# Performance work log

Hardware: AMD Instinct MI355X
Metric: run time of the kernel (lower is better)

## Reference

```python
import jax, jax.numpy as jnp
import numpy as np

LOG2PI = float(np.log(2.0 * np.pi))
BN_EPS = 1e-5


def _spn_layer(x, scopes, mean, std, sum_w, bn_w, bn_b):
    """Vectorized SPNLayer of SPNNeurons.
    x:      [B, F]
    scopes: [O, F] int, per-neuron permutation of feature indices
    mean/std: [O, F//2, n_mv, 2] gaussian leaf params (pairs of features)
    sum_w:  [O, F//2, n_mv] sum-node mixture weights (softmax-normalized)
    bn_w, bn_b: [O] batchnorm affine params (training-mode batch stats)
    returns [B, O]
    """
    B = x.shape[0]
    O, P, M, _ = mean.shape
    # gather permuted features and group into pairs: [B, O, P, 2]
    xp = x[:, scopes].reshape(B, O, P, 2)
    # gaussian leaf log-likelihoods: [B, O, P, M, 2]
    z = (xp[:, :, :, None, :] - mean) / std
    ll = -0.5 * (z * z) - jnp.log(std) - 0.5 * LOG2PI
    # product node over each pair: [B, O, P, M]
    prod = ll.sum(axis=-1)
    # sum node: weighted mixture in log domain: [B, O, P]
    logw = jax.nn.log_softmax(sum_w, axis=-1)
    s = jax.nn.logsumexp(prod + logw, axis=-1)
    # root product node over all pairs: [B, O]
    out = s.sum(axis=-1)
    # BatchNorm1d (training mode, biased variance)
    mu = out.mean(axis=0)
    var = ((out - mu) ** 2).mean(axis=0)
    return (out - mu) / jnp.sqrt(var + BN_EPS) * bn_w + bn_b


def setup_inputs() -> dict:
    key = jax.random.key(0)
    ks = jax.random.split(key, 12)
    B, F_IN = 32768, 784
    H1, O1, O2, OUT = 32, 16, 10, 10
    n_mv = 2

    rng = np.random.RandomState(0)
    scopes1 = jnp.asarray(np.stack([rng.permutation(H1) for _ in range(O1)]), dtype=jnp.int32)
    scopes2 = jnp.asarray(np.stack([rng.permutation(O1) for _ in range(O2)]), dtype=jnp.int32)

    x = jax.random.normal(ks[0], (B, F_IN), jnp.float32)
    W1 = jax.random.normal(ks[1], (H1, F_IN), jnp.float32) * np.sqrt(2.0 / F_IN)
    b1 = jnp.zeros((H1,), jnp.float32)

    mean1 = jax.random.normal(ks[2], (O1, H1 // 2, n_mv, 2), jnp.float32)
    std1 = jax.random.uniform(ks[3], (O1, H1 // 2, n_mv, 2), jnp.float32, 0.5, 1.5)
    sw1 = jax.random.uniform(ks[4], (O1, H1 // 2, n_mv), jnp.float32)
    bn1_w = jnp.ones((O1,), jnp.float32)
    bn1_b = jnp.zeros((O1,), jnp.float32)

    mean2 = jax.random.normal(ks[5], (O2, O1 // 2, n_mv, 2), jnp.float32)
    std2 = jax.random.uniform(ks[6], (O2, O1 // 2, n_mv, 2), jnp.float32, 0.5, 1.5)
    sw2 = jax.random.uniform(ks[7], (O2, O1 // 2, n_mv), jnp.float32)
    bn2_w = jnp.ones((O2,), jnp.float32)
    bn2_b = jnp.zeros((O2,), jnp.float32)

    W2 = jax.random.normal(ks[8], (OUT, O2), jnp.float32) * np.sqrt(2.0 / O2)
    b2 = jnp.zeros((OUT,), jnp.float32)

    return {"x": x, "W1": W1, "b1": b1,
            "mean1": mean1, "std1": std1, "sw1": sw1, "bn1_w": bn1_w, "bn1_b": bn1_b,
            "mean2": mean2, "std2": std2, "sw2": sw2, "bn2_w": bn2_w, "bn2_b": bn2_b,
            "W2": W2, "b2": b2, "scopes1": scopes1, "scopes2": scopes2}


def reference(x, W1, b1, mean1, std1, sw1, bn1_w, bn1_b,
              mean2, std2, sw2, bn2_w, bn2_b, W2, b2, scopes1, scopes2):
    h = jax.nn.relu(x @ W1.T + b1)                                  # [B, 32]
    h = _spn_layer(h, scopes1, mean1, std1, sw1, bn1_w, bn1_b)      # [B, 16]
    h = _spn_layer(h, scopes2, mean2, std2, sw2, bn2_w, bn2_b)      # [B, 10]
    logits = h @ W2.T + b2                                          # [B, 10]
    return jax.nn.log_softmax(logits, axis=1)
```

## Files before the change

### kernel.cpp

```cpp
#include <hip/hip_runtime.h>
#include <hip/hip_bf16.h>
#include <math.h>

#define LOG2PI_F 1.8378770664093453f
#define BN_EPS 1e-5f
#define BATCH 32768

#define K1_ROWS 64
#define NB1 (BATCH / K1_ROWS)
#define WS1 840
#define NB3 1024
#define RPB3 32

typedef __attribute__((ext_vector_type(8))) short bf16x8;
typedef __attribute__((ext_vector_type(4))) float f32x4;

__device__ __forceinline__ short f2bf_s(float f) {
    union { __hip_bfloat16 b; short s; } u;
    u.b = __float2bfloat16(f);
    return u.s;
}
__device__ __forceinline__ float bfs_to_f(short s) {
    return __uint_as_float(((unsigned)(unsigned short)s) << 16);
}

__global__ __launch_bounds__(256) void k0_cvt(
    const float* __restrict__ W1, __hip_bfloat16* __restrict__ w1h,
    __hip_bfloat16* __restrict__ w1l)
{
    int i = blockIdx.x * 256 + threadIdx.x;
    if (i >= 32 * WS1) return;
    int o = i / WS1, k = i - o * WS1;
    float w = (k < 784) ? W1[o * 784 + k] : 0.f;
    __hip_bfloat16 h = __float2bfloat16(w);
    float hf = __bfloat162float(h);
    __hip_bfloat16 l = __float2bfloat16(w - hf);
    w1h[i] = h;
    w1l[i] = l;
}

struct Step { float4 a0, a1; bf16x8 wh0, wl0, wh1, wl1; };

__device__ __forceinline__ void load_step(
    Step& S, const float* __restrict__ xrow,
    const __hip_bfloat16* __restrict__ wh, const __hip_bfloat16* __restrict__ wl,
    int s, int kgrp, int o0)
{
    int kb = s * 32 + kgrp * 8;
    int kc = (kb < 784) ? kb : 0;
    S.a0 = *(const float4*)(xrow + kc);
    S.a1 = *(const float4*)(xrow + kc + 4);
    const __hip_bfloat16* ph = wh + o0 * WS1 + kb;
    const __hip_bfloat16* pl = wl + o0 * WS1 + kb;
    S.wh0 = *(const bf16x8*)(ph);
    S.wh1 = *(const bf16x8*)(ph + 16 * WS1);
    S.wl0 = *(const bf16x8*)(pl);
    S.wl1 = *(const bf16x8*)(pl + 16 * WS1);
}

__device__ __forceinline__ void comp_step(const Step& S, f32x4& acc0, f32x4& acc1)
{
    float av[8] = {S.a0.x, S.a0.y, S.a0.z, S.a0.w, S.a1.x, S.a1.y, S.a1.z, S.a1.w};
    bf16x8 ah, al;
    #pragma unroll
    for (int e = 0; e < 8; ++e) {
        float f = av[e];
        short h = f2bf_s(f);
        ah[e] = h;
        al[e] = f2bf_s(f - bfs_to_f(h));
    }
    acc0 = __builtin_amdgcn_mfma_f32_16x16x32_bf16(ah, S.wh0, acc0, 0, 0, 0);
    acc0 = __builtin_amdgcn_mfma_f32_16x16x32_bf16(al, S.wh0, acc0, 0, 0, 0);
    acc0 = __builtin_amdgcn_mfma_f32_16x16x32_bf16(ah, S.wl0, acc0, 0, 0, 0);
    acc1 = __builtin_amdgcn_mfma_f32_16x16x32_bf16(ah, S.wh1, acc1, 0, 0, 0);
    acc1 = __builtin_amdgcn_mfma_f32_16x16x32_bf16(al, S.wh1, acc1, 0, 0, 0);
    acc1 = __builtin_amdgcn_mfma_f32_16x16x32_bf16(ah, S.wl1, acc1, 0, 0, 0);
}

__global__ __launch_bounds__(256, 2) void k1_gemm_spn1(
    const float* __restrict__ x,
    const __hip_bfloat16* __restrict__ w1h, const __hip_bfloat16* __restrict__ w1l,
    const float* __restrict__ b1,
    const float* __restrict__ mean1, const float* __restrict__ std1, const float* __restrict__ sw1,
    const int* __restrict__ scopes1,
    float* __restrict__ s1, float* __restrict__ partials1)
{
    __shared__ float h_lds[64][33];
    __shared__ float mu_l[1024], inv_l[1024], c0_l[512];
    __shared__ int   sc_l[512];
    __shared__ float b1_l[32];
    __shared__ float sv_l[16][66];

    const int t = threadIdx.x;

    for (int il = t; il < 1024; il += 256) {
        int o = il & 15, rest = il >> 4;
        int f = rest & 1, m = (rest >> 1) & 1, p = rest >> 2;
        int ig = ((o * 16 + p) * 2 + m) * 2 + f;
        mu_l[il]  = mean1[ig];
        inv_l[il] = 1.0f / std1[ig];
    }
    for (int il = t; il < 512; il += 256) {
        int o = il & 15, rest = il >> 4;
        int m = rest & 1, p = rest >> 1;
        int igw = (o * 16 + p) * 2;
        float w0 = sw1[igw], w1v = sw1[igw + 1];
        float mx = fmaxf(w0, w1v);
        float lse = mx + __logf(__expf(w0 - mx) + __expf(w1v - mx));
        float wm = (m == 0) ? w0 : w1v;
        int igs = ((o * 16 + p) * 2 + m) * 2;
        c0_l[il] = (wm - lse) - __logf(std1[igs]) - __logf(std1[igs + 1]) - LOG2PI_F;
    }
    for (int il = t; il < 512; il += 256) sc_l[il] = scopes1[il];
    if (t < 32) b1_l[t] = b1[t];

    const int wid  = t >> 6;
    const int lane = t & 63;
    const int row0 = blockIdx.x * K1_ROWS;
    const int kgrp = (lane >> 4) & 3;
    const int o0   = lane & 15;
    const float* xrow = x + (size_t)(row0 + wid * 16 + (lane & 15)) * 784;

    f32x4 acc0 = {0.f, 0.f, 0.f, 0.f};
    f32x4 acc1 = {0.f, 0.f, 0.f, 0.f};

    Step A0, A1, A2, B0, B1, B2;
    load_step(A0, xrow, w1h, w1l, 0, kgrp, o0);
    load_step(A1, xrow, w1h, w1l, 1, kgrp, o0);
    load_step(A2, xrow, w1h, w1l, 2, kgrp, o0);
    #pragma unroll
    for (int gg = 0; gg < 4; ++gg) {
        int g0 = gg * 6;
        load_step(B0, xrow, w1h, w1l, g0 + 3, kgrp, o0);
        load_step(B1, xrow, w1h, w1l, g0 + 4, kgrp, o0);
        load_step(B2, xrow, w1h, w1l, g0 + 5, kgrp, o0);
        comp_step(A0, acc0, acc1);
        comp_step(A1, acc0, acc1);
        comp_step(A2, acc0, acc1);
        if (gg < 3) {
            load_step(A0, xrow, w1h, w1l, g0 + 6, kgrp, o0);
            load_step(A1, xrow, w1h, w1l, g0 + 7, kgrp, o0);
            load_step(A2, xrow, w1h, w1l, g0 + 8, kgrp, o0);
        }
        comp_step(B0, acc0, acc1);
        comp_step(B1, acc0, acc1);
        comp_step(B2, acc0, acc1);
    }
    {
        Step T;
        load_step(T, xrow, w1h, w1l, 24, kgrp, o0);
        comp_step(T, acc0, acc1);
    }

    __syncthreads();

    {
        int col = lane & 15;
        int rbase = wid * 16 + ((lane >> 4) & 3) * 4;
        #pragma unroll
        for (int r = 0; r < 4; ++r) {
            h_lds[rbase + r][col]      = fmaxf(acc0[r] + b1_l[col], 0.f);
            h_lds[rbase + r][16 + col] = fmaxf(acc1[r] + b1_l[16 + col], 0.f);
        }
    }
    __syncthreads();

    for (int task = t; task < 1024; task += 256) {
        int row_l = task >> 4, o = task & 15;
        float outv = 0.f;
        for (int p = 0; p < 16; ++p) {
            int f0 = sc_l[o * 32 + 2 * p], f1 = sc_l[o * 32 + 2 * p + 1];
            float x0 = h_lds[row_l][f0];
            float x1 = h_lds[row_l][f1];
            float vm[2];
            #pragma unroll
            for (int m = 0; m < 2; ++m) {
                int base = ((p * 2 + m) * 2) * 16 + o;
                float d0 = (x0 - mu_l[base])      * inv_l[base];
                float d1 = (x1 - mu_l[base + 16]) * inv_l[base + 16];
                vm[m] = c0_l[(p * 2 + m) * 16 + o] - 0.5f * (d0 * d0 + d1 * d1);
            }
            float a  = fmaxf(vm[0], vm[1]);
            float bm = fminf(vm[0], vm[1]);
            outv += a + __logf(1.f + __expf(bm - a));
        }
        s1[(size_t)(row0 + row_l) * 16 + o] = outv;
        sv_l[o][row_l] = outv;
    }
    __syncthreads();

    if (t < 16) {
        float s = 0.f;
        for (int rr = 0; rr < K1_ROWS; ++rr) s += sv_l[t][rr];
        float mb = s * (1.f / K1_ROWS);
        float m2 = 0.f;
        for (int rr = 0; rr < K1_ROWS; ++rr) { float d = sv_l[t][rr] - mb; m2 += d * d; }
        partials1[blockIdx.x * 32 + t]      = s;
        partials1[blockIdx.x * 32 + 16 + t] = m2;
    }
}

template <int NO, int NBLK, int RPB>
__global__ __launch_bounds__(256) void kreduce(
    const float* __restrict__ partials,
    const float* __restrict__ bn_w, const float* __restrict__ bn_b,
    float* __restrict__ stats)
{
    __shared__ double dsum[256];
    __shared__ double dmean[16];
    const int t = threadIdx.x;
    const int o = t & 15, seg = t >> 4;
    const int per = NBLK / 16;

    double s = 0.0;
    if (o < NO)
        for (int b = seg * per; b < (seg + 1) * per; ++b)
            s += (double)partials[b * (2 * NO) + o];
    dsum[t] = s;
    __syncthreads();
    if (t < 16) {
        double S = 0.0;
        for (int g = 0; g < 16; ++g) S += dsum[g * 16 + t];
        dmean[t] = S / (double)BATCH;
    }
    __syncthreads();
    double mean = dmean[o];
    double m2 = 0.0;
    if (o < NO) {
        for (int b = seg * per; b < (seg + 1) * per; ++b) {
            double bm = (double)partials[b * (2 * NO) + o] / (double)RPB;
            double d  = bm - mean;
            m2 += (double)partials[b * (2 * NO) + NO + o] + (double)RPB * d * d;
        }
    }
    __syncthreads();
    dsum[t] = m2;
    __syncthreads();
    if (t < NO) {
        double M2 = 0.0;
        for (int g = 0; g < 16; ++g) M2 += dsum[g * 16 + t];
        double var = M2 / (double)BATCH;
        double gsc = (double)bn_w[t] / sqrt(var + (double)BN_EPS);
        stats[t]      = (float)gsc;
        stats[NO + t] = (float)((double)bn_b[t] - dmean[t] * gsc);
    }
}

__global__ __launch_bounds__(320, 4) void k3_spn2(
    const float* __restrict__ s1,
    const float* __restrict__ mean2, const float* __restrict__ std2, const float* __restrict__ sw2,
    const int* __restrict__ scopes2, const float* __restrict__ stats1,
    float* __restrict__ s2, float* __restrict__ partials2)
{
    __shared__ float mu_l[320], inv_l[320], c0_l[160];
    __shared__ int   sc_l[160];
    __shared__ float v_lds[32][17];
    __shared__ float sv_l[10][33];
    __shared__ float g_l[16], sh_l[16];

    const int t = threadIdx.x;
    const int row0 = blockIdx.x * RPB3;

    if (t < 320) {
        int o = t % 10, rest = t / 10;
        int f = rest & 1, m = (rest >> 1) & 1, p = rest >> 2;
        int ig = ((o * 8 + p) * 2 + m) * 2 + f;
        mu_l[t]  = mean2[ig];
        inv_l[t] = 1.0f / std2[ig];
    }
    if (t < 160) {
        int o = t % 10, rest = t / 10;
        int m = rest & 1, p = rest >> 1;
        int igw = (o * 8 + p) * 2;
        float w0 = sw2[igw], w1 = sw2[igw + 1];
        float mx = fmaxf(w0, w1);
        float lse = mx + __logf(__expf(w0 - mx) + __expf(w1 - mx));
        float wm = (m == 0) ? w0 : w1;
        int igs = ((o * 8 + p) * 2 + m) * 2;
        c0_l[t] = (wm - lse) - __logf(std2[igs]) - __logf(std2[igs + 1]) - LOG2PI_F;
    }
    if (t < 160) sc_l[t] = scopes2[t];
    if (t < 16)  g_l[t]  = stats1[t];
    else if (t >= 64 && t < 80) sh_l[t - 64] = stats1[16 + (t - 64)];
    __syncthreads();

    for (int i = t; i < 512; i += 320) {
        int rl = i >> 4, f = i & 15;
        v_lds[rl][f] = fmaf(s1[(size_t)(row0 + rl) * 16 + f], g_l[f], sh_l[f]);
    }
    __syncthreads();

    const int row_l = t / 10, o = t % 10;
    float outv = 0.f;
    for (int p = 0; p < 8; ++p) {
        int f0 = sc_l[o * 16 + 2 * p], f1 = sc_l[o * 16 + 2 * p + 1];
        float x0 = v_lds[row_l][f0], x1 = v_lds[row_l][f1];
        float vm[2];
        #pragma unroll
        for (int m = 0; m < 2; ++m) {
            int base = ((p * 2 + m) * 2) * 10 + o;
            float d0 = (x0 - mu_l[base])      * inv_l[base];
            float d1 = (x1 - mu_l[base + 10]) * inv_l[base + 10];
            vm[m] = c0_l[(p * 2 + m) * 10 + o] - 0.5f * (d0 * d0 + d1 * d1);
        }
        float a  = fmaxf(vm[0], vm[1]);
        float bm = fminf(vm[0], vm[1]);
        outv += a + __logf(1.f + __expf(bm - a));
    }
    s2[(size_t)(row0 + row_l) * 10 + o] = outv;
    sv_l[o][row_l] = outv;
    __syncthreads();

    if (t < 10) {
        float s = 0.f;
        for (int rr = 0; rr < RPB3; ++rr) s += sv_l[t][rr];
        float mb = s * (1.f / RPB3);
        float m2 = 0.f;
        for (int rr = 0; rr < RPB3; ++rr) { float d = sv_l[t][rr] - mb; m2 += d * d; }
        partials2[blockIdx.x * 20 + t]      = s;
        partials2[blockIdx.x * 20 + 10 + t] = m2;
    }
}

__global__ __launch_bounds__(128) void k5_head(
    const float* __restrict__ s2, const float* __restrict__ stats2,
    const float* __restrict__ W2, const float* __restrict__ b2,
    float* __restrict__ out)
{
    __shared__ float w2_l[100], b2_l[10], st_l[20];
    const int t = threadIdx.x;
    if (t < 100) w2_l[t] = W2[t];
    if (t < 10)  b2_l[t] = b2[t];
    if (t < 20)  st_l[t] = stats2[t];
    __syncthreads();

    const int row = blockIdx.x * 128 + t;
    const float* sr = s2 + (size_t)row * 10;
    float v[10], l[10];
    #pragma unroll
    for (int i = 0; i < 5; ++i) {
        float2 p = *(const float2*)(sr + 2 * i);
        v[2*i]   = fmaf(p.x, st_l[2*i],   st_l[10 + 2*i]);
        v[2*i+1] = fmaf(p.y, st_l[2*i+1], st_l[10 + 2*i+1]);
    }
    float mx = -1e30f;
    #pragma unroll
    for (int c = 0; c < 10; ++c) {
        float a = b2_l[c];
        #pragma unroll
        for (int o = 0; o < 10; ++o) a = fmaf(w2_l[c * 10 + o], v[o], a);
        l[c] = a;
        mx = fmaxf(mx, a);
    }
    float sum = 0.f;
    #pragma unroll
    for (int c = 0; c < 10; ++c) sum += __expf(l[c] - mx);
    float ls = mx + __logf(sum);
    float* orow = out + (size_t)row * 10;
    #pragma unroll
    for (int c = 0; c < 10; ++c) orow[c] = l[c] - ls;
}

extern "C" void kernel_launch(void* const* d_in, const int* in_sizes, int n_in,
                              void* d_out, int out_size, void* d_ws, size_t ws_size,
                              hipStream_t stream) {
    const float* x      = (const float*)d_in[0];
    const float* W1     = (const float*)d_in[1];
    const float* b1     = (const float*)d_in[2];
    const float* mean1  = (const float*)d_in[3];
    const float* std1   = (const float*)d_in[4];
    const float* sw1    = (const float*)d_in[5];
    const float* bn1_w  = (const float*)d_in[6];
    const float* bn1_b  = (const float*)d_in[7];
    const float* mean2  = (const float*)d_in[8];
    const float* std2   = (const float*)d_in[9];
    const float* sw2    = (const float*)d_in[10];
    const float* bn2_w  = (const float*)d_in[11];
    const float* bn2_b  = (const float*)d_in[12];
    const float* W2     = (const float*)d_in[13];
    const float* b2     = (const float*)d_in[14];
    const int*   sc1    = (const int*)d_in[15];
    const int*   sc2    = (const int*)d_in[16];
    float* out = (float*)d_out;

    __hip_bfloat16* w1h = (__hip_bfloat16*)d_ws;
    __hip_bfloat16* w1l = w1h + 32 * WS1;
    float* fbase = (float*)(w1l + 32 * WS1);
    float* s1  = fbase;
    float* s2  = s1 + 32768 * 16;
    float* p1  = s2 + 32768 * 10;
    float* p2  = p1 + NB1 * 32;
    float* st1 = p2 + NB3 * 20;
    float* st2 = st1 + 32;

    hipLaunchKernelGGL(k0_cvt, dim3((32 * WS1 + 255) / 256), dim3(256), 0, stream,
                       W1, w1h, w1l);
    hipLaunchKernelGGL(k1_gemm_spn1, dim3(NB1), dim3(256), 0, stream,
                       x, w1h, w1l, b1, mean1, std1, sw1, sc1, s1, p1);
    hipLaunchKernelGGL((kreduce<16, NB1, K1_ROWS>), dim3(1), dim3(256), 0, stream, p1, bn1_w, bn1_b, st1);
    hipLaunchKernelGGL(k3_spn2, dim3(NB3), dim3(320), 0, stream,
                       s1, mean2, std2, sw2, sc2, st1, s2, p2);
    hipLaunchKernelGGL((kreduce<10, NB3, RPB3>), dim3(1), dim3(256), 0, stream, p2, bn2_w, bn2_b, st2);
    hipLaunchKernelGGL(k5_head, dim3(BATCH / 128), dim3(128), 0, stream,
                       s2, st2, W2, b2, out);
}
```

Baseline: 236.3 us.

## Fold batchnorm stat reductions into consumer kernels and shrink GEMM blocks

Removes the two single-block kreduce launches. Every k3_spn2 block and every k5_head block now recomputes the batchnorm mean, variance, scale and shift from the partials in double precision. k1 is reworked to 32-row, 128-thread blocks with a shallower two-stage, non-unrolled load/compute loop, and k5_head now uses 256-thread blocks. This saves launch and serialization cost, but each consumer block now re-reads the whole partials array and runs serial double loops. The less deeply prefetched GEMM loop may also hide memory latency less well.

Measured after the change: 267.2 us. +13.1%, slower.

```diff
diff --git a/kernel.cpp b/kernel.cpp
--- a/kernel.cpp
+++ b/kernel.cpp
@@ -6,7 +6,7 @@
 #define BN_EPS 1e-5f
 #define BATCH 32768
 
-#define K1_ROWS 64
+#define K1_ROWS 32
 #define NB1 (BATCH / K1_ROWS)
 #define WS1 840
 #define NB3 1024
@@ -77,7 +77,7 @@
     acc1 = __builtin_amdgcn_mfma_f32_16x16x32_bf16(ah, S.wl1, acc1, 0, 0, 0);
 }
 
-__global__ __launch_bounds__(256, 2) void k1_gemm_spn1(
+__global__ __launch_bounds__(128, 4) void k1_gemm_spn1(
     const float* __restrict__ x,
     const __hip_bfloat16* __restrict__ w1h, const __hip_bfloat16* __restrict__ w1l,
     const float* __restrict__ b1,
@@ -85,22 +85,22 @@
     const int* __restrict__ scopes1,
     float* __restrict__ s1, float* __restrict__ partials1)
 {
-    __shared__ float h_lds[64][33];
+    __shared__ float h_lds[32][33];
     __shared__ float mu_l[1024], inv_l[1024], c0_l[512];
     __shared__ int   sc_l[512];
     __shared__ float b1_l[32];
-    __shared__ float sv_l[16][66];
+    __shared__ float sv_l[16][33];
 
     const int t = threadIdx.x;
 
-    for (int il = t; il < 1024; il += 256) {
+    for (int il = t; il < 1024; il += 128) {
         int o = il & 15, rest = il >> 4;
         int f = rest & 1, m = (rest >> 1) & 1, p = rest >> 2;
         int ig = ((o * 16 + p) * 2 + m) * 2 + f;
         mu_l[il]  = mean1[ig];
         inv_l[il] = 1.0f / std1[ig];
     }
-    for (int il = t; il < 512; il += 256) {
+    for (int il = t; il < 512; il += 128) {
         int o = il & 15, rest = il >> 4;
         int m = rest & 1, p = rest >> 1;
         int igw = (o * 16 + p) * 2;
@@ -111,7 +111,7 @@
         int igs = ((o * 16 + p) * 2 + m) * 2;
         c0_l[il] = (wm - lse) - __logf(std1[igs]) - __logf(std1[igs + 1]) - LOG2PI_F;
     }
-    for (int il = t; il < 512; il += 256) sc_l[il] = scopes1[il];
+    for (int il = t; il < 512; il += 128) sc_l[il] = scopes1[il];
     if (t < 32) b1_l[t] = b1[t];
 
     const int wid  = t >> 6;
@@ -124,39 +124,22 @@
     f32x4 acc0 = {0.f, 0.f, 0.f, 0.f};
     f32x4 acc1 = {0.f, 0.f, 0.f, 0.f};
 
-    Step A0, A1, A2, B0, B1, B2;
-    load_step(A0, xrow, w1h, w1l, 0, kgrp, o0);
-    load_step(A1, xrow, w1h, w1l, 1, kgrp, o0);
-    load_step(A2, xrow, w1h, w1l, 2, kgrp, o0);
-    #pragma unroll
-    for (int gg = 0; gg < 4; ++gg) {
-        int g0 = gg * 6;
-        load_step(B0, xrow, w1h, w1l, g0 + 3, kgrp, o0);
-        load_step(B1, xrow, w1h, w1l, g0 + 4, kgrp, o0);
-        load_step(B2, xrow, w1h, w1l, g0 + 5, kgrp, o0);
-        comp_step(A0, acc0, acc1);
-        comp_step(A1, acc0, acc1);
-        comp_step(A2, acc0, acc1);
-        if (gg < 3) {
-            load_step(A0, xrow, w1h, w1l, g0 + 6, kgrp, o0);
-            load_step(A1, xrow, w1h, w1l, g0 + 7, kgrp, o0);
-            load_step(A2, xrow, w1h, w1l, g0 + 8, kgrp, o0);
-        }
-        comp_step(B0, acc0, acc1);
-        comp_step(B1, acc0, acc1);
-        comp_step(B2, acc0, acc1);
-    }
-    {
-        Step T;
-        load_step(T, xrow, w1h, w1l, 24, kgrp, o0);
-        comp_step(T, acc0, acc1);
-    }
+    Step SA, SB;
+    load_step(SA, xrow, w1h, w1l, 0, kgrp, o0);
+    #pragma unroll 1
+    for (int pp = 0; pp < 12; ++pp) {
+        load_step(SB, xrow, w1h, w1l, 2 * pp + 1, kgrp, o0);
+        comp_step(SA, acc0, acc1);
+        load_step(SA, xrow, w1h, w1l, 2 * pp + 2, kgrp, o0);
+        comp_step(SB, acc0, acc1);
+    }
+    comp_step(SA, acc0, acc1);
 
     __syncthreads();
 
     {
         int col = lane & 15;
-        int rbase = wid * 16 + ((lane >> 4) & 3) * 4;
+        int rbase = wid * 16 + kgrp * 4;
         #pragma unroll
         for (int r = 0; r < 4; ++r) {
             h_lds[rbase + r][col]      = fmaxf(acc0[r] + b1_l[col], 0.f);
@@ -165,7 +148,7 @@
     }
     __syncthreads();
 
-    for (int task = t; task < 1024; task += 256) {
+    for (int task = t; task < 512; task += 128) {
         int row_l = task >> 4, o = task & 15;
         float outv = 0.f;
         for (int p = 0; p < 16; ++p) {
@@ -200,56 +183,11 @@
     }
 }
 
-template <int NO, int NBLK, int RPB>
-__global__ __launch_bounds__(256) void kreduce(
-    const float* __restrict__ partials,
-    const float* __restrict__ bn_w, const float* __restrict__ bn_b,
-    float* __restrict__ stats)
-{
-    __shared__ double dsum[256];
-    __shared__ double dmean[16];
-    const int t = threadIdx.x;
-    const int o = t & 15, seg = t >> 4;
-    const int per = NBLK / 16;
-
-    double s = 0.0;
-    if (o < NO)
-        for (int b = seg * per; b < (seg + 1) * per; ++b)
-            s += (double)partials[b * (2 * NO) + o];
-    dsum[t] = s;
-    __syncthreads();
-    if (t < 16) {
-        double S = 0.0;
-        for (int g = 0; g < 16; ++g) S += dsum[g * 16 + t];
-        dmean[t] = S / (double)BATCH;
-    }
-    __syncthreads();
-    double mean = dmean[o];
-    double m2 = 0.0;
-    if (o < NO) {
-        for (int b = seg * per; b < (seg + 1) * per; ++b) {
-            double bm = (double)partials[b * (2 * NO) + o] / (double)RPB;
-            double d  = bm - mean;
-            m2 += (double)partials[b * (2 * NO) + NO + o] + (double)RPB * d * d;
-        }
-    }
-    __syncthreads();
-    dsum[t] = m2;
-    __syncthreads();
-    if (t < NO) {
-        double M2 = 0.0;
-        for (int g = 0; g < 16; ++g) M2 += dsum[g * 16 + t];
-        double var = M2 / (double)BATCH;
-        double gsc = (double)bn_w[t] / sqrt(var + (double)BN_EPS);
-        stats[t]      = (float)gsc;
-        stats[NO + t] = (float)((double)bn_b[t] - dmean[t] * gsc);
-    }
-}
-
 __global__ __launch_bounds__(320, 4) void k3_spn2(
-    const float* __restrict__ s1,
+    const float* __restrict__ s1, const float* __restrict__ partials1,
+    const float* __restrict__ bn1_w, const float* __restrict__ bn1_b,
     const float* __restrict__ mean2, const float* __restrict__ std2, const float* __restrict__ sw2,
-    const int* __restrict__ scopes2, const float* __restrict__ stats1,
+    const int* __restrict__ scopes2,
     float* __restrict__ s2, float* __restrict__ partials2)
 {
     __shared__ float mu_l[320], inv_l[320], c0_l[160];
@@ -257,6 +195,8 @@
     __shared__ float v_lds[32][17];
     __shared__ float sv_l[10][33];
     __shared__ float g_l[16], sh_l[16];
+    __shared__ double dsum[256];
+    __shared__ double dmean[16];
 
     const int t = threadIdx.x;
     const int row0 = blockIdx.x * RPB3;
@@ -280,8 +220,46 @@
         c0_l[t] = (wm - lse) - __logf(std2[igs]) - __logf(std2[igs + 1]) - LOG2PI_F;
     }
     if (t < 160) sc_l[t] = scopes2[t];
-    if (t < 16)  g_l[t]  = stats1[t];
-    else if (t >= 64 && t < 80) sh_l[t - 64] = stats1[16 + (t - 64)];
+
+    {
+        const int o = t & 15, seg = t >> 4;
+        const int per = NB1 / 16;
+        if (t < 256) {
+            double s = 0.0;
+            for (int b = seg * per; b < (seg + 1) * per; ++b)
+                s += (double)partials1[b * 32 + o];
+            dsum[t] = s;
+        }
+        __syncthreads();
+        if (t < 16) {
+            double S = 0.0;
+            for (int g = 0; g < 16; ++g) S += dsum[g * 16 + t];
+            dmean[t] = S / (double)BATCH;
+        }
+        __syncthreads();
+        if (t < 256) {
+            double mean = dmean[o];
+            double m2 = 0.0;
+            for (int b = seg * per; b < (seg + 1) * per; ++b) {
+                double bm = (double)partials1[b * 32 + o] / (double)K1_ROWS;
+                double d  = bm - mean;
+                m2 += (double)partials1[b * 32 + 16 + o] + (double)K1_ROWS * d * d;
+            }
+            __syncthreads();
+            dsum[t] = m2;
+        } else {
+            __syncthreads();
+        }
+        __syncthreads();
+        if (t < 16) {
+            double M2 = 0.0;
+            for (int g = 0; g < 16; ++g) M2 += dsum[g * 16 + t];
+            double var = M2 / (double)BATCH;
+            double gsc = (double)bn1_w[t] / sqrt(var + (double)BN_EPS);
+            g_l[t]  = (float)gsc;
+            sh_l[t] = (float)((double)bn1_b[t] - dmean[t] * gsc);
+        }
+    }
     __syncthreads();
 
     for (int i = t; i < 512; i += 320) {
@@ -322,19 +300,58 @@
     }
 }
 
-__global__ __launch_bounds__(128) void k5_head(
-    const float* __restrict__ s2, const float* __restrict__ stats2,
+__global__ __launch_bounds__(256) void k5_head(
+    const float* __restrict__ s2, const float* __restrict__ partials2,
+    const float* __restrict__ bn2_w, const float* __restrict__ bn2_b,
     const float* __restrict__ W2, const float* __restrict__ b2,
     float* __restrict__ out)
 {
     __shared__ float w2_l[100], b2_l[10], st_l[20];
+    __shared__ double dsum[256];
+    __shared__ double dmean[16];
     const int t = threadIdx.x;
     if (t < 100) w2_l[t] = W2[t];
-    if (t < 10)  b2_l[t] = b2[t];
-    if (t < 20)  st_l[t] = stats2[t];
-    __syncthreads();
-
-    const int row = blockIdx.x * 128 + t;
+    if (t >= 128 && t < 138) b2_l[t - 128] = b2[t - 128];
+
+    {
+        const int o = t & 15, seg = t >> 4;
+        const int per = NB3 / 16;
+        double s = 0.0;
+        if (o < 10)
+            for (int b = seg * per; b < (seg + 1) * per; ++b)
+                s += (double)partials2[b * 20 + o];
+        dsum[t] = s;
+        __syncthreads();
+        if (t < 16) {
+            double S = 0.0;
+            for (int g = 0; g < 16; ++g) S += dsum[g * 16 + t];
+            dmean[t] = S / (double)BATCH;
+        }
+        __syncthreads();
+        double mean = dmean[o];
+        double m2 = 0.0;
+        if (o < 10) {
+            for (int b = seg * per; b < (seg + 1) * per; ++b) {
+                double bm = (double)partials2[b * 20 + o] / (double)RPB3;
+                double d  = bm - mean;
+                m2 += (double)partials2[b * 20 + 10 + o] + (double)RPB3 * d * d;
+            }
+        }
+        __syncthreads();
+        dsum[t] = m2;
+        __syncthreads();
+        if (t < 10) {
+            double M2 = 0.0;
+            for (int g = 0; g < 16; ++g) M2 += dsum[g * 16 + t];
+            double var = M2 / (double)BATCH;
+            double gsc = (double)bn2_w[t] / sqrt(var + (double)BN_EPS);
+            st_l[t]      = (float)gsc;
+            st_l[10 + t] = (float)((double)bn2_b[t] - dmean[t] * gsc);
+        }
+    }
+    __syncthreads();
+
+    const int row = blockIdx.x * 256 + t;
     const float* sr = s2 + (size_t)row * 10;
     float v[10], l[10];
     #pragma unroll
@@ -390,17 +407,13 @@
     float* s2  = s1 + 32768 * 16;
     float* p1  = s2 + 32768 * 10;
     float* p2  = p1 + NB1 * 32;
-    float* st1 = p2 + NB3 * 20;
-    float* st2 = st1 + 32;
 
     hipLaunchKernelGGL(k0_cvt, dim3((32 * WS1 + 255) / 256), dim3(256), 0, stream,
                        W1, w1h, w1l);
-    hipLaunchKernelGGL(k1_gemm_spn1, dim3(NB1), dim3(256), 0, stream,
+    hipLaunchKernelGGL(k1_gemm_spn1, dim3(NB1), dim3(128), 0, stream,
                        x, w1h, w1l, b1, mean1, std1, sw1, sc1, s1, p1);
-    hipLaunchKernelGGL((kreduce<16, NB1, K1_ROWS>), dim3(1), dim3(256), 0, stream, p1, bn1_w, bn1_b, st1);
     hipLaunchKernelGGL(k3_spn2, dim3(NB3), dim3(320), 0, stream,
-                       s1, mean2, std2, sw2, sc2, st1, s2, p2);
-    hipLaunchKernelGGL((kreduce<10, NB3, RPB3>), dim3(1), dim3(256), 0, stream, p2, bn2_w, bn2_b, st2);
-    hipLaunchKernelGGL(k5_head, dim3(BATCH / 128), dim3(128), 0, stream,
-                       s2, st2, W2, b2, out);
-}
+                       s1, p1, bn1_w, bn1_b, mean2, std2, sw2, sc2, s2, p2);
+    hipLaunchKernelGGL(k5_head, dim3(BATCH / 256), dim3(256), 0, stream,
+                       s2, p2, bn2_w, bn2_b, W2, b2, out);
+}
```
